# Kernel tuning notes

Measured on AMD Instinct MI355X. Metric: run time of the kernel, lower is better.

Reference implementation:

```python
import jax, jax.numpy as jnp
import numpy as np

B, U, D, N, O = 128, 16, 256, 1024, 256
RES_CONN, IN_CONN, BIAS_P = 0.2, 0.2, 0.5


def _fixed_bernoulli(rng, heads, rows, cols, conn):
    # each column has exactly nb = int(conn*rows) ones (as in the torch code)
    nb = max(1, int(conn * rows))
    r = rng.random((heads, rows, cols))
    thr = np.sort(r, axis=1)[:, nb - 1:nb, :]
    return (r <= thr).astype(np.float32)


def setup_inputs() -> dict:
    rng = np.random.default_rng(0)
    # recurrent weights: normal * fixed-bernoulli mask, normalized by spectral radius
    W = rng.normal(size=(U, N, N)).astype(np.float32) * _fixed_bernoulli(rng, U, N, N, RES_CONN)
    sr0 = np.abs(np.linalg.eigvals(W.astype(np.float64))).max(axis=-1).astype(np.float32).reshape(U, 1, 1)
    W = W / sr0
    Win = _fixed_bernoulli(rng, U, D, N, IN_CONN)
    bias = (rng.random((U, 1, N)) < BIAS_P).astype(np.float32)
    Wout = rng.normal(size=(U, N, O)).astype(np.float32)
    adaptive_lr = rng.random((U, D, 1)).astype(np.float32)
    sr = rng.random((U, 1, 1)).astype(np.float32)
    temperature = np.ones((1,), np.float32)
    X = rng.normal(size=(B, U, D)).astype(np.float32)
    state = rng.normal(size=(B, U, N)).astype(np.float32)
    arrs = dict(X=X, state=state, W=W, Win=Win, bias=bias, Wout=Wout,
                sr=sr, adaptive_lr=adaptive_lr, temperature=temperature)
    return {k: jnp.asarray(v) for k, v in arrs.items()}


def reference(X, state, W, Win, bias, Wout, sr, adaptive_lr, temperature):
    # X: [B,U,D] -> [B,U,1,D]; state: [B,U,N] -> [B,U,1,N]
    x = X[:, :, None, :]
    s = state[:, :, None, :]
    # adaptive per-unit learning rate: softmax over the units axis
    lr = jax.nn.softmax(jnp.einsum('buid,udk->buik', x, adaptive_lr) / temperature, axis=1)  # [B,U,1,1]
    feed = jnp.einsum('buid,udn->buin', x, Win)            # [B,U,1,N]
    echo = jnp.einsum('buin,unm->buim', s, W * sr) + bias  # [B,U,1,N]
    new_state = (1.0 - lr) * s + lr * jnp.tanh(feed + echo)
    output = jnp.einsum('buin,uno->buio', new_state, Wout)  # [B,U,1,O]
    return new_state[:, :, 0, :], output[:, :, 0, :]
```

## Files before the change

### kernel.cpp

```cpp
#include <hip/hip_runtime.h>
#include <math.h>

#define Bsz 128
#define Usz 16
#define Dsz 256
#define Nsz 1024
#define Osz 256

typedef __attribute__((ext_vector_type(4))) float f32x4;
typedef __attribute__((ext_vector_type(8))) short bf16x8;

__device__ __forceinline__ unsigned short f2bf(float f) {
    union { float f; unsigned int u; } v; v.f = f;
    unsigned int lsb = (v.u >> 16) & 1u;
    v.u += 0x7fffu + lsb;
    return (unsigned short)(v.u >> 16);
}

__device__ __forceinline__ bf16x8 pack8(const float* x, float s) {
    union { bf16x8 v; unsigned short h[8]; } r;
    #pragma unroll
    for (int i = 0; i < 8; i++) r.h[i] = f2bf(x[i] * s);
    return r.v;
}

__global__ __launch_bounds__(256)
void lr_kernel(const float* __restrict__ X, const float* __restrict__ alr,
               const float* __restrict__ temp, float* __restrict__ lr)
{
    const int b = blockIdx.x;
    const int t = threadIdx.x;
    const int u = t >> 4;
    const int l = t & 15;
    const float* xp = X + ((size_t)b * Usz + u) * Dsz;
    const float* ap = alr + (size_t)u * Dsz;
    float s = 0.f;
    for (int d = l; d < Dsz; d += 16) s += xp[d] * ap[d];
    s += __shfl_down(s, 8, 16);
    s += __shfl_down(s, 4, 16);
    s += __shfl_down(s, 2, 16);
    s += __shfl_down(s, 1, 16);
    __shared__ float logits[16];
    if (l == 0) logits[u] = s;
    __syncthreads();
    if (t < 16) {
        const float T = temp[0];
        float m = -1e30f;
        #pragma unroll
        for (int i = 0; i < 16; i++) m = fmaxf(m, logits[i] / T);
        float sum = 0.f;
        #pragma unroll
        for (int i = 0; i < 16; i++) sum += expf(logits[i] / T - m);
        lr[(size_t)b * Usz + t] = expf(logits[t] / T - m) / sum;
    }
}

__global__ __launch_bounds__(256)
void state_mfma(const float* __restrict__ X, const float* __restrict__ state,
                const float* __restrict__ W, const float* __restrict__ Win,
                const float* __restrict__ bias, const float* __restrict__ sr,
                const float* __restrict__ lr, float* __restrict__ out0)
{
    const int id = blockIdx.x;
    const int mt = id >> 8;
    const int rr = id & 255;
    const int u  = (rr & 7) | ((rr >> 7) << 3);
    const int nt = (rr >> 3) & 15;

    const int tid  = threadIdx.x;
    const int wave = tid >> 6, lane = tid & 63;
    const int l16  = lane & 15, kgl = lane >> 4;
    const int wrow = (wave & 1) * 32, wcol = (wave >> 1) * 32;

    __shared__ __align__(16) unsigned short As[64 * 32];
    __shared__ __align__(16) unsigned short Bs[64 * 32];

    f32x4 acc[2][2] = {};

    const int sm  = tid & 63;
    const int skg = tid >> 6;
    const float sru = sr[u];

    const float* Af = X     + ((size_t)(mt * 64 + sm) * Usz + u) * Dsz + skg * 8;
    const float* Ae = state + ((size_t)(mt * 64 + sm) * Usz + u) * Nsz + skg * 8;
    const float* Bf = Win + (size_t)u * Dsz * Nsz + (size_t)(skg * 8) * Nsz + nt * 64 + sm;
    const float* Be = W   + (size_t)u * Nsz * Nsz + (size_t)(skg * 8) * Nsz + nt * 64 + sm;

    float areg[8], breg[8];

    auto loadA = [&](int kb) {
        const float* p = (kb < Dsz) ? (Af + kb) : (Ae + (kb - Dsz));
        const f32x4 v0 = *(const f32x4*)p;
        const f32x4 v1 = *(const f32x4*)(p + 4);
        #pragma unroll
        for (int i = 0; i < 4; i++) { areg[i] = v0[i]; areg[4 + i] = v1[i]; }
    };
    auto loadB = [&](int kb) {
        const float* p = (kb < Dsz) ? (Bf + (size_t)kb * Nsz)
                                    : (Be + (size_t)(kb - Dsz) * Nsz);
        #pragma unroll
        for (int j = 0; j < 8; j++) breg[j] = p[(size_t)j * Nsz];
    };

    loadA(0); loadB(0);
    const int wr_off = ((sm >> 4) * 4 + skg) * 128 + (sm & 15) * 8;

    for (int step = 0; step < 40; ++step) {
        const int kb = step * 32;
        const float asc = (kb < Dsz) ? 1.f : sru;
        const bf16x8 av = pack8(areg, asc);
        const bf16x8 bv = pack8(breg, 1.f);
        __syncthreads();
        *(bf16x8*)&As[wr_off] = av;
        *(bf16x8*)&Bs[wr_off] = bv;
        __syncthreads();
        if (step + 1 < 40) { loadA(kb + 32); loadB(kb + 32); }
        bf16x8 afr[2], bfr[2];
        #pragma unroll
        for (int mi = 0; mi < 2; mi++)
            afr[mi] = *(const bf16x8*)&As[((((wrow >> 4) + mi) * 4 + kgl) * 16 + l16) * 8];
        #pragma unroll
        for (int ni = 0; ni < 2; ni++)
            bfr[ni] = *(const bf16x8*)&Bs[((((wcol >> 4) + ni) * 4 + kgl) * 16 + l16) * 8];
        #pragma unroll
        for (int mi = 0; mi < 2; mi++)
            #pragma unroll
            for (int ni = 0; ni < 2; ni++)
                acc[mi][ni] = __builtin_amdgcn_mfma_f32_16x16x32_bf16(afr[mi], bfr[ni], acc[mi][ni], 0, 0, 0);
    }

    #pragma unroll
    for (int mi = 0; mi < 2; mi++) {
        #pragma unroll
        for (int ni = 0; ni < 2; ni++) {
            const int gcol = nt * 64 + wcol + ni * 16 + l16;
            const float bi = bias[u * Nsz + gcol];
            #pragma unroll
            for (int rg = 0; rg < 4; rg++) {
                const int grow = mt * 64 + wrow + mi * 16 + kgl * 4 + rg;
                const size_t idx = ((size_t)grow * Usz + u) * Nsz + gcol;
                const float th = tanhf(acc[mi][ni][rg] + bi);
                const float sv = state[idx];
                const float lv = lr[grow * Usz + u];
                out0[idx] = (1.f - lv) * sv + lv * th;
            }
        }
    }
}

__global__ __launch_bounds__(256)
void out_mfma(const float* __restrict__ ns, const float* __restrict__ Wout,
              float* __restrict__ out1)
{
    const int id = blockIdx.x;
    const int u  = (id & 7) | ((id >> 7) << 3);
    const int mt = (id >> 3) & 3;
    const int ot = (id >> 5) & 3;

    const int tid  = threadIdx.x;
    const int wave = tid >> 6, lane = tid & 63;
    const int l16  = lane & 15, kgl = lane >> 4;
    const int wrow = (wave & 1) * 16, wcol = (wave >> 1) * 32;

    __shared__ __align__(16) unsigned short As[32 * 32];
    __shared__ __align__(16) unsigned short Bs[64 * 32];

    f32x4 acc[2] = {};

    const int sa_m = tid & 31, sa_kg = (tid >> 5) & 3;
    const int sb_n = tid & 63, sb_kg = tid >> 6;

    const float* Ap = ns + ((size_t)(mt * 32 + sa_m) * Usz + u) * Nsz + sa_kg * 8;
    const float* Bp = Wout + (size_t)u * Nsz * Osz + (size_t)(sb_kg * 8) * Osz + ot * 64 + sb_n;

    float areg[8], breg[8];
    auto loadA = [&](int kb) {
        if (tid < 128) {
            const f32x4 v0 = *(const f32x4*)(Ap + kb);
            const f32x4 v1 = *(const f32x4*)(Ap + kb + 4);
            #pragma unroll
            for (int i = 0; i < 4; i++) { areg[i] = v0[i]; areg[4 + i] = v1[i]; }
        }
    };
    auto loadB = [&](int kb) {
        const float* p = Bp + (size_t)kb * Osz;
        #pragma unroll
        for (int j = 0; j < 8; j++) breg[j] = p[(size_t)j * Osz];
    };

    loadA(0); loadB(0);
    const int wa_off = ((sa_m >> 4) * 4 + sa_kg) * 128 + (sa_m & 15) * 8;
    const int wb_off = ((sb_n >> 4) * 4 + sb_kg) * 128 + (sb_n & 15) * 8;

    for (int step = 0; step < 32; ++step) {
        const int kb = step * 32;
        bf16x8 av = pack8(areg, 1.f);
        const bf16x8 bv = pack8(breg, 1.f);
        __syncthreads();
        if (tid < 128) *(bf16x8*)&As[wa_off] = av;
        *(bf16x8*)&Bs[wb_off] = bv;
        __syncthreads();
        if (step + 1 < 32) { loadA(kb + 32); loadB(kb + 32); }
        const bf16x8 afr = *(const bf16x8*)&As[(((wave & 1) * 4 + kgl) * 16 + l16) * 8];
        bf16x8 bfr[2];
        #pragma unroll
        for (int ni = 0; ni < 2; ni++)
            bfr[ni] = *(const bf16x8*)&Bs[((((wcol >> 4) + ni) * 4 + kgl) * 16 + l16) * 8];
        #pragma unroll
        for (int ni = 0; ni < 2; ni++)
            acc[ni] = __builtin_amdgcn_mfma_f32_16x16x32_bf16(afr, bfr[ni], acc[ni], 0, 0, 0);
    }

    #pragma unroll
    for (int ni = 0; ni < 2; ni++) {
        const int gcol = ot * 64 + wcol + ni * 16 + l16;
        #pragma unroll
        for (int rg = 0; rg < 4; rg++) {
            const int grow = mt * 32 + wrow + kgl * 4 + rg;
            out1[((size_t)grow * Usz + u) * Osz + gcol] = acc[ni][rg];
        }
    }
}

extern "C" void kernel_launch(void* const* d_in, const int* in_sizes, int n_in,
                              void* d_out, int out_size, void* d_ws, size_t ws_size,
                              hipStream_t stream)
{
    (void)in_sizes; (void)n_in; (void)out_size; (void)ws_size;
    const float* X     = (const float*)d_in[0];
    const float* state = (const float*)d_in[1];
    const float* W     = (const float*)d_in[2];
    const float* Win   = (const float*)d_in[3];
    const float* bias  = (const float*)d_in[4];
    const float* Wout  = (const float*)d_in[5];
    const float* sr    = (const float*)d_in[6];
    const float* alr   = (const float*)d_in[7];
    const float* temp  = (const float*)d_in[8];

    float* out0 = (float*)d_out;
    float* out1 = out0 + (size_t)Bsz * Usz * Nsz;
    float* lr   = (float*)d_ws;

    lr_kernel<<<Bsz, 256, 0, stream>>>(X, alr, temp, lr);
    state_mfma<<<512, 256, 0, stream>>>(X, state, W, Win, bias, sr, lr, out0);
    out_mfma<<<256, 256, 0, stream>>>(out0, Wout, out1);
}
```

Measured before the change: 202.9 us.

## Double-buffer LDS tiles and halve M tiles to double grid size

Both MFMA GEMM kernels now use double-buffered shared memory with a two-deep register prefetch, so each step needs one barrier instead of two and global loads overlap the MFMAs. The M tile is halved (64→32 rows in the state kernel, 32→16 in the output kernel), which doubles the block count to 1024 and 512 to fill more CUs. Block-index mapping changes so units vary fastest. The trade-off is that weight tiles are re-read from global/L2 by twice as many blocks, and each wave does less MFMA work per loaded tile.

```diff
diff --git a/kernel.cpp b/kernel.cpp
--- a/kernel.cpp
+++ b/kernel.cpp
@@ -61,126 +61,128 @@
                 const float* __restrict__ bias, const float* __restrict__ sr,
                 const float* __restrict__ lr, float* __restrict__ out0)
 {
-    const int id = blockIdx.x;
-    const int mt = id >> 8;
-    const int rr = id & 255;
-    const int u  = (rr & 7) | ((rr >> 7) << 3);
-    const int nt = (rr >> 3) & 15;
-
-    const int tid  = threadIdx.x;
-    const int wave = tid >> 6, lane = tid & 63;
-    const int l16  = lane & 15, kgl = lane >> 4;
-    const int wrow = (wave & 1) * 32, wcol = (wave >> 1) * 32;
-
-    __shared__ __align__(16) unsigned short As[64 * 32];
-    __shared__ __align__(16) unsigned short Bs[64 * 32];
-
-    f32x4 acc[2][2] = {};
-
-    const int sm  = tid & 63;
-    const int skg = tid >> 6;
-    const float sru = sr[u];
-
-    const float* Af = X     + ((size_t)(mt * 64 + sm) * Usz + u) * Dsz + skg * 8;
-    const float* Ae = state + ((size_t)(mt * 64 + sm) * Usz + u) * Nsz + skg * 8;
-    const float* Bf = Win + (size_t)u * Dsz * Nsz + (size_t)(skg * 8) * Nsz + nt * 64 + sm;
-    const float* Be = W   + (size_t)u * Nsz * Nsz + (size_t)(skg * 8) * Nsz + nt * 64 + sm;
-
-    float areg[8], breg[8];
-
-    auto loadA = [&](int kb) {
-        const float* p = (kb < Dsz) ? (Af + kb) : (Ae + (kb - Dsz));
-        const f32x4 v0 = *(const f32x4*)p;
-        const f32x4 v1 = *(const f32x4*)(p + 4);
-        #pragma unroll
-        for (int i = 0; i < 4; i++) { areg[i] = v0[i]; areg[4 + i] = v1[i]; }
-    };
-    auto loadB = [&](int kb) {
-        const float* p = (kb < Dsz) ? (Bf + (size_t)kb * Nsz)
-                                    : (Be + (size_t)(kb - Dsz) * Nsz);
-        #pragma unroll
-        for (int j = 0; j < 8; j++) breg[j] = p[(size_t)j * Nsz];
-    };
-
-    loadA(0); loadB(0);
-    const int wr_off = ((sm >> 4) * 4 + skg) * 128 + (sm & 15) * 8;
-
-    for (int step = 0; step < 40; ++step) {
-        const int kb = step * 32;
-        const float asc = (kb < Dsz) ? 1.f : sru;
-        const bf16x8 av = pack8(areg, asc);
-        const bf16x8 bv = pack8(breg, 1.f);
-        __syncthreads();
-        *(bf16x8*)&As[wr_off] = av;
-        *(bf16x8*)&Bs[wr_off] = bv;
-        __syncthreads();
-        if (step + 1 < 40) { loadA(kb + 32); loadB(kb + 32); }
-        bf16x8 afr[2], bfr[2];
-        #pragma unroll
-        for (int mi = 0; mi < 2; mi++)
-            afr[mi] = *(const bf16x8*)&As[((((wrow >> 4) + mi) * 4 + kgl) * 16 + l16) * 8];
-        #pragma unroll
-        for (int ni = 0; ni < 2; ni++)
-            bfr[ni] = *(const bf16x8*)&Bs[((((wcol >> 4) + ni) * 4 + kgl) * 16 + l16) * 8];
-        #pragma unroll
-        for (int mi = 0; mi < 2; mi++)
-            #pragma unroll
-            for (int ni = 0; ni < 2; ni++)
-                acc[mi][ni] = __builtin_amdgcn_mfma_f32_16x16x32_bf16(afr[mi], bfr[ni], acc[mi][ni], 0, 0, 0);
-    }
-
-    #pragma unroll
-    for (int mi = 0; mi < 2; mi++) {
-        #pragma unroll
-        for (int ni = 0; ni < 2; ni++) {
-            const int gcol = nt * 64 + wcol + ni * 16 + l16;
-            const float bi = bias[u * Nsz + gcol];
-            #pragma unroll
-            for (int rg = 0; rg < 4; rg++) {
-                const int grow = mt * 64 + wrow + mi * 16 + kgl * 4 + rg;
-                const size_t idx = ((size_t)grow * Usz + u) * Nsz + gcol;
-                const float th = tanhf(acc[mi][ni][rg] + bi);
-                const float sv = state[idx];
-                const float lv = lr[grow * Usz + u];
-                out0[idx] = (1.f - lv) * sv + lv * th;
-            }
-        }
-    }
-}
-
-__global__ __launch_bounds__(256)
-void out_mfma(const float* __restrict__ ns, const float* __restrict__ Wout,
-              float* __restrict__ out1)
-{
-    const int id = blockIdx.x;
-    const int u  = (id & 7) | ((id >> 7) << 3);
-    const int mt = (id >> 3) & 3;
-    const int ot = (id >> 5) & 3;
+    const int id   = blockIdx.x;
+    const int u    = id & 15;
+    const int rest = id >> 4;
+    const int nt   = rest & 15;
+    const int mt   = rest >> 4;
 
     const int tid  = threadIdx.x;
     const int wave = tid >> 6, lane = tid & 63;
     const int l16  = lane & 15, kgl = lane >> 4;
     const int wrow = (wave & 1) * 16, wcol = (wave >> 1) * 32;
 
-    __shared__ __align__(16) unsigned short As[32 * 32];
-    __shared__ __align__(16) unsigned short Bs[64 * 32];
+    __shared__ __align__(16) unsigned short As[2][1024];
+    __shared__ __align__(16) unsigned short Bs[2][2048];
 
     f32x4 acc[2] = {};
 
-    const int sa_m = tid & 31, sa_kg = (tid >> 5) & 3;
-    const int sb_n = tid & 63, sb_kg = tid >> 6;
-
-    const float* Ap = ns + ((size_t)(mt * 32 + sa_m) * Usz + u) * Nsz + sa_kg * 8;
-    const float* Bp = Wout + (size_t)u * Nsz * Osz + (size_t)(sb_kg * 8) * Osz + ot * 64 + sb_n;
+    const int  sm  = tid & 31;
+    const int  skg = (tid >> 5) & 3;
+    const bool doA = tid < 128;
+    const int  sb_n = tid & 63, sb_kg = tid >> 6;
+    const float sru = sr[u];
+
+    const float* Af = X     + ((size_t)(mt * 32 + sm) * Usz + u) * Dsz + skg * 8;
+    const float* Ae = state + ((size_t)(mt * 32 + sm) * Usz + u) * Nsz + skg * 8;
+    const float* Bf = Win + (size_t)u * Dsz * Nsz + (size_t)(sb_kg * 8) * Nsz + nt * 64 + sb_n;
+    const float* Be = W   + (size_t)u * Nsz * Nsz + (size_t)(sb_kg * 8) * Nsz + nt * 64 + sb_n;
 
     float areg[8], breg[8];
     auto loadA = [&](int kb) {
-        if (tid < 128) {
-            const f32x4 v0 = *(const f32x4*)(Ap + kb);
-            const f32x4 v1 = *(const f32x4*)(Ap + kb + 4);
-            #pragma unroll
-            for (int i = 0; i < 4; i++) { areg[i] = v0[i]; areg[4 + i] = v1[i]; }
+        if (!doA) return;
+        const float* p = (kb < Dsz) ? (Af + kb) : (Ae + (kb - Dsz));
+        const f32x4 v0 = *(const f32x4*)p;
+        const f32x4 v1 = *(const f32x4*)(p + 4);
+        #pragma unroll
+        for (int i = 0; i < 4; i++) { areg[i] = v0[i]; areg[4 + i] = v1[i]; }
+    };
+    auto loadB = [&](int kb) {
+        const float* p = (kb < Dsz) ? (Bf + (size_t)kb * Nsz)
+                                    : (Be + (size_t)(kb - Dsz) * Nsz);
+        #pragma unroll
+        for (int j = 0; j < 8; j++) breg[j] = p[(size_t)j * Nsz];
+    };
+
+    const int wrA = ((sm >> 4) * 4 + skg) * 128 + (sm & 15) * 8;
+    const int wrB = ((sb_n >> 4) * 4 + sb_kg) * 128 + (sb_n & 15) * 8;
+    auto writeBuf = [&](int buf, int kb) {
+        const float asc = (kb < Dsz) ? 1.f : sru;
+        if (doA) *(bf16x8*)&As[buf][wrA] = pack8(areg, asc);
+        *(bf16x8*)&Bs[buf][wrB] = pack8(breg, 1.f);
+    };
+
+    loadA(0); loadB(0);
+    writeBuf(0, 0);
+    loadA(32); loadB(32);
+    __syncthreads();
+
+    const int aoff  = (((wave & 1) * 4 + kgl) * 16 + l16) * 8;
+    const int boff0 = ((((wcol >> 4) + 0) * 4 + kgl) * 16 + l16) * 8;
+    const int boff1 = ((((wcol >> 4) + 1) * 4 + kgl) * 16 + l16) * 8;
+
+    for (int step = 0; step < 40; ++step) {
+        const int buf = step & 1;
+        if (step + 1 < 40) writeBuf(buf ^ 1, (step + 1) * 32);
+        if (step + 2 < 40) { loadA((step + 2) * 32); loadB((step + 2) * 32); }
+        const bf16x8 afr = *(const bf16x8*)&As[buf][aoff];
+        const bf16x8 b0  = *(const bf16x8*)&Bs[buf][boff0];
+        const bf16x8 b1  = *(const bf16x8*)&Bs[buf][boff1];
+        acc[0] = __builtin_amdgcn_mfma_f32_16x16x32_bf16(afr, b0, acc[0], 0, 0, 0);
+        acc[1] = __builtin_amdgcn_mfma_f32_16x16x32_bf16(afr, b1, acc[1], 0, 0, 0);
+        __syncthreads();
+    }
+
+    #pragma unroll
+    for (int ni = 0; ni < 2; ni++) {
+        const int gcol = nt * 64 + wcol + ni * 16 + l16;
+        const float bi = bias[u * Nsz + gcol];
+        #pragma unroll
+        for (int rg = 0; rg < 4; rg++) {
+            const int grow = mt * 32 + wrow + kgl * 4 + rg;
+            const size_t idx = ((size_t)grow * Usz + u) * Nsz + gcol;
+            const float th = tanhf(acc[ni][rg] + bi);
+            const float sv = state[idx];
+            const float lv = lr[grow * Usz + u];
+            out0[idx] = (1.f - lv) * sv + lv * th;
         }
+    }
+}
+
+__global__ __launch_bounds__(256)
+void out_mfma(const float* __restrict__ ns, const float* __restrict__ Wout,
+              float* __restrict__ out1)
+{
+    const int id   = blockIdx.x;
+    const int u    = id & 15;
+    const int rest = id >> 4;
+    const int ot   = rest & 3;
+    const int mt   = rest >> 2;
+
+    const int tid  = threadIdx.x;
+    const int wave = tid >> 6, lane = tid & 63;
+    const int l16  = lane & 15, kgl = lane >> 4;
+    const int wcol = wave * 16;
+
+    __shared__ __align__(16) unsigned short As[2][512];
+    __shared__ __align__(16) unsigned short Bs[2][2048];
+
+    f32x4 acc = {};
+
+    const bool doA = tid < 64;
+    const int  sm  = tid & 15, skg = (tid >> 4) & 3;
+    const int  sb_n = tid & 63, sb_kg = tid >> 6;
+
+    const float* Ap = ns + ((size_t)(mt * 16 + sm) * Usz + u) * Nsz + skg * 8;
+    const float* Bp = Wout + (size_t)u * Nsz * Osz + (size_t)(sb_kg * 8) * Osz + ot * 64 + sb_n;
+
+    float areg[8], breg[8];
+    auto loadA = [&](int kb) {
+        if (!doA) return;
+        const f32x4 v0 = *(const f32x4*)(Ap + kb);
+        const f32x4 v1 = *(const f32x4*)(Ap + kb + 4);
+        #pragma unroll
+        for (int i = 0; i < 4; i++) { areg[i] = v0[i]; areg[4 + i] = v1[i]; }
     };
     auto loadB = [&](int kb) {
         const float* p = Bp + (size_t)kb * Osz;
@@ -188,37 +190,36 @@
         for (int j = 0; j < 8; j++) breg[j] = p[(size_t)j * Osz];
     };
 
+    const int wrA = skg * 128 + sm * 8;
+    const int wrB = ((sb_n >> 4) * 4 + sb_kg) * 128 + (sb_n & 15) * 8;
+    auto writeBuf = [&](int buf) {
+        if (doA) *(bf16x8*)&As[buf][wrA] = pack8(areg, 1.f);
+        *(bf16x8*)&Bs[buf][wrB] = pack8(breg, 1.f);
+    };
+
     loadA(0); loadB(0);
-    const int wa_off = ((sa_m >> 4) * 4 + sa_kg) * 128 + (sa_m & 15) * 8;
-    const int wb_off = ((sb_n >> 4) * 4 + sb_kg) * 128 + (sb_n & 15) * 8;
+    writeBuf(0);
+    loadA(32); loadB(32);
+    __syncthreads();
+
+    const int aoff = (kgl * 16 + l16) * 8;
+    const int boff = ((wave * 4 + kgl) * 16 + l16) * 8;
 
     for (int step = 0; step < 32; ++step) {
-        const int kb = step * 32;
-        bf16x8 av = pack8(areg, 1.f);
-        const bf16x8 bv = pack8(breg, 1.f);
+        const int buf = step & 1;
+        if (step + 1 < 32) writeBuf(buf ^ 1);
+        if (step + 2 < 32) { loadA((step + 2) * 32); loadB((step + 2) * 32); }
+        const bf16x8 afr = *(const bf16x8*)&As[buf][aoff];
+        const bf16x8 bfr = *(const bf16x8*)&Bs[buf][boff];
+        acc = __builtin_amdgcn_mfma_f32_16x16x32_bf16(afr, bfr, acc, 0, 0, 0);
         __syncthreads();
-        if (tid < 128) *(bf16x8*)&As[wa_off] = av;
-        *(bf16x8*)&Bs[wb_off] = bv;
-        __syncthreads();
-        if (step + 1 < 32) { loadA(kb + 32); loadB(kb + 32); }
-        const bf16x8 afr = *(const bf16x8*)&As[(((wave & 1) * 4 + kgl) * 16 + l16) * 8];
-        bf16x8 bfr[2];
-        #pragma unroll
-        for (int ni = 0; ni < 2; ni++)
-            bfr[ni] = *(const bf16x8*)&Bs[((((wcol >> 4) + ni) * 4 + kgl) * 16 + l16) * 8];
-        #pragma unroll
-        for (int ni = 0; ni < 2; ni++)
-            acc[ni] = __builtin_amdgcn_mfma_f32_16x16x32_bf16(afr, bfr[ni], acc[ni], 0, 0, 0);
-    }
-
+    }
+
+    const int gcol = ot * 64 + wcol + l16;
     #pragma unroll
-    for (int ni = 0; ni < 2; ni++) {
-        const int gcol = ot * 64 + wcol + ni * 16 + l16;
-        #pragma unroll
-        for (int rg = 0; rg < 4; rg++) {
-            const int grow = mt * 32 + wrow + kgl * 4 + rg;
-            out1[((size_t)grow * Usz + u) * Osz + gcol] = acc[ni][rg];
-        }
+    for (int rg = 0; rg < 4; rg++) {
+        const int grow = mt * 16 + kgl * 4 + rg;
+        out1[((size_t)grow * Usz + u) * Osz + gcol] = acc[rg];
     }
 }
 
@@ -242,6 +243,6 @@
     float* lr   = (float*)d_ws;
 
     lr_kernel<<<Bsz, 256, 0, stream>>>(X, alr, temp, lr);
-    state_mfma<<<512, 256, 0, stream>>>(X, state, W, Win, bias, sr, lr, out0);
-    out_mfma<<<256, 256, 0, stream>>>(out0, Wout, out1);
-}
+    state_mfma<<<1024, 256, 0, stream>>>(X, state, W, Win, bias, sr, lr, out0);
+    out_mfma<<<512, 256, 0, stream>>>(out0, Wout, out1);
+}
```

New measurement: 203.8 us. No clear change (+0.4%).

## Drop LDS staging in GEMM kernels, load MFMA fragments directly from global memory

Applied to the files above, without the earlier changes.

Both MFMA kernels no longer stage tiles through shared memory with two barriers per step. Each wave now loads its own A/B fragments from global memory into double-buffered registers, and conversion to bf16 becomes truncation via byte permute instead of round-to-nearest. Block-to-tile mapping changes: state_mfma puts unit in the low bits, and out_mfma gives each wave its own 16x16 tile across twice as many blocks. This removes barrier and LDS traffic but duplicates global loads across waves, and truncation lowers precision slightly.

```diff
diff --git a/kernel.cpp b/kernel.cpp
--- a/kernel.cpp
+++ b/kernel.cpp
@@ -9,19 +9,24 @@
 
 typedef __attribute__((ext_vector_type(4))) float f32x4;
 typedef __attribute__((ext_vector_type(8))) short bf16x8;
-
-__device__ __forceinline__ unsigned short f2bf(float f) {
-    union { float f; unsigned int u; } v; v.f = f;
-    unsigned int lsb = (v.u >> 16) & 1u;
-    v.u += 0x7fffu + lsb;
-    return (unsigned short)(v.u >> 16);
-}
-
-__device__ __forceinline__ bf16x8 pack8(const float* x, float s) {
-    union { bf16x8 v; unsigned short h[8]; } r;
+typedef __attribute__((ext_vector_type(4))) unsigned int u32x4;
+
+union cell_u { u32x4 u; bf16x8 b; };
+
+__device__ __forceinline__ unsigned int fbits(float f) {
+    union { float f; unsigned int u; } v; v.f = f; return v.u;
+}
+__device__ __forceinline__ unsigned int pk(float lo, float hi) {
+    return __builtin_amdgcn_perm(fbits(hi), fbits(lo), 0x07060302u);
+}
+__device__ __forceinline__ bf16x8 pk8s(const float* x, float s) {
+    float t[8];
     #pragma unroll
-    for (int i = 0; i < 8; i++) r.h[i] = f2bf(x[i] * s);
-    return r.v;
+    for (int i = 0; i < 8; i++) t[i] = x[i] * s;
+    cell_u r;
+    r.u[0] = pk(t[0], t[1]); r.u[1] = pk(t[2], t[3]);
+    r.u[2] = pk(t[4], t[5]); r.u[3] = pk(t[6], t[7]);
+    return r.b;
 }
 
 __global__ __launch_bounds__(256)
@@ -55,89 +60,93 @@
     }
 }
 
-__global__ __launch_bounds__(256)
+__global__ __launch_bounds__(256, 2)
 void state_mfma(const float* __restrict__ X, const float* __restrict__ state,
                 const float* __restrict__ W, const float* __restrict__ Win,
                 const float* __restrict__ bias, const float* __restrict__ sr,
                 const float* __restrict__ lr, float* __restrict__ out0)
 {
     const int id = blockIdx.x;
+    const int u  = id & 15;
+    const int nt = (id >> 4) & 15;
     const int mt = id >> 8;
-    const int rr = id & 255;
-    const int u  = (rr & 7) | ((rr >> 7) << 3);
-    const int nt = (rr >> 3) & 15;
 
     const int tid  = threadIdx.x;
     const int wave = tid >> 6, lane = tid & 63;
     const int l16  = lane & 15, kgl = lane >> 4;
-    const int wrow = (wave & 1) * 32, wcol = (wave >> 1) * 32;
-
-    __shared__ __align__(16) unsigned short As[64 * 32];
-    __shared__ __align__(16) unsigned short Bs[64 * 32];
+    const int wm = wave & 1, wn = wave >> 1;
+
+    const int row0 = mt * 64 + wm * 32 + l16;
+    const int col0 = nt * 64 + wn * 32 + l16;
+
+    const float sru = sr[u];
+
+    const float* Ax0 = X + ((size_t)row0 * Usz + u) * Dsz;
+    const float* Ax1 = X + ((size_t)(row0 + 16) * Usz + u) * Dsz;
+    const float* Ae0 = state + ((size_t)row0 * Usz + u) * Nsz;
+    const float* Ae1 = state + ((size_t)(row0 + 16) * Usz + u) * Nsz;
+    const float* Bf  = Win + (size_t)u * Dsz * Nsz + col0;
+    const float* Be  = W   + (size_t)u * Nsz * Nsz + col0;
+
+    float a[2][2][8];
+    float b[2][2][8];
+
+    auto loadStep = [&](int step, int buf) {
+        const int kb = step * 32 + kgl * 8;
+        if (kb < Dsz) {
+            *(f32x4*)&a[buf][0][0] = *(const f32x4*)(Ax0 + kb);
+            *(f32x4*)&a[buf][0][4] = *(const f32x4*)(Ax0 + kb + 4);
+            *(f32x4*)&a[buf][1][0] = *(const f32x4*)(Ax1 + kb);
+            *(f32x4*)&a[buf][1][4] = *(const f32x4*)(Ax1 + kb + 4);
+            const float* bp = Bf + (size_t)kb * Nsz;
+            #pragma unroll
+            for (int j = 0; j < 8; j++) {
+                b[buf][0][j] = bp[(size_t)j * Nsz];
+                b[buf][1][j] = bp[(size_t)j * Nsz + 16];
+            }
+        } else {
+            const int kk = kb - Dsz;
+            *(f32x4*)&a[buf][0][0] = *(const f32x4*)(Ae0 + kk);
+            *(f32x4*)&a[buf][0][4] = *(const f32x4*)(Ae0 + kk + 4);
+            *(f32x4*)&a[buf][1][0] = *(const f32x4*)(Ae1 + kk);
+            *(f32x4*)&a[buf][1][4] = *(const f32x4*)(Ae1 + kk + 4);
+            const float* bp = Be + (size_t)kk * Nsz;
+            #pragma unroll
+            for (int j = 0; j < 8; j++) {
+                b[buf][0][j] = bp[(size_t)j * Nsz];
+                b[buf][1][j] = bp[(size_t)j * Nsz + 16];
+            }
+        }
+    };
 
     f32x4 acc[2][2] = {};
-
-    const int sm  = tid & 63;
-    const int skg = tid >> 6;
-    const float sru = sr[u];
-
-    const float* Af = X     + ((size_t)(mt * 64 + sm) * Usz + u) * Dsz + skg * 8;
-    const float* Ae = state + ((size_t)(mt * 64 + sm) * Usz + u) * Nsz + skg * 8;
-    const float* Bf = Win + (size_t)u * Dsz * Nsz + (size_t)(skg * 8) * Nsz + nt * 64 + sm;
-    const float* Be = W   + (size_t)u * Nsz * Nsz + (size_t)(skg * 8) * Nsz + nt * 64 + sm;
-
-    float areg[8], breg[8];
-
-    auto loadA = [&](int kb) {
-        const float* p = (kb < Dsz) ? (Af + kb) : (Ae + (kb - Dsz));
-        const f32x4 v0 = *(const f32x4*)p;
-        const f32x4 v1 = *(const f32x4*)(p + 4);
-        #pragma unroll
-        for (int i = 0; i < 4; i++) { areg[i] = v0[i]; areg[4 + i] = v1[i]; }
-    };
-    auto loadB = [&](int kb) {
-        const float* p = (kb < Dsz) ? (Bf + (size_t)kb * Nsz)
-                                    : (Be + (size_t)(kb - Dsz) * Nsz);
-        #pragma unroll
-        for (int j = 0; j < 8; j++) breg[j] = p[(size_t)j * Nsz];
-    };
-
-    loadA(0); loadB(0);
-    const int wr_off = ((sm >> 4) * 4 + skg) * 128 + (sm & 15) * 8;
+    loadStep(0, 0);
 
     for (int step = 0; step < 40; ++step) {
-        const int kb = step * 32;
-        const float asc = (kb < Dsz) ? 1.f : sru;
-        const bf16x8 av = pack8(areg, asc);
-        const bf16x8 bv = pack8(breg, 1.f);
-        __syncthreads();
-        *(bf16x8*)&As[wr_off] = av;
-        *(bf16x8*)&Bs[wr_off] = bv;
-        __syncthreads();
-        if (step + 1 < 40) { loadA(kb + 32); loadB(kb + 32); }
-        bf16x8 afr[2], bfr[2];
+        const int cur = step & 1;
+        if (step + 1 < 40) loadStep(step + 1, cur ^ 1);
+        const float asc = (step < 8) ? 1.f : sru;
+        bf16x8 af[2], bf[2];
+        af[0] = pk8s(a[cur][0], asc);
+        af[1] = pk8s(a[cur][1], asc);
+        bf[0] = pk8s(b[cur][0], 1.f);
+        bf[1] = pk8s(b[cur][1], 1.f);
         #pragma unroll
         for (int mi = 0; mi < 2; mi++)
-            afr[mi] = *(const bf16x8*)&As[((((wrow >> 4) + mi) * 4 + kgl) * 16 + l16) * 8];
-        #pragma unroll
-        for (int ni = 0; ni < 2; ni++)
-            bfr[ni] = *(const bf16x8*)&Bs[((((wcol >> 4) + ni) * 4 + kgl) * 16 + l16) * 8];
-        #pragma unroll
-        for (int mi = 0; mi < 2; mi++)
             #pragma unroll
             for (int ni = 0; ni < 2; ni++)
-                acc[mi][ni] = __builtin_amdgcn_mfma_f32_16x16x32_bf16(afr[mi], bfr[ni], acc[mi][ni], 0, 0, 0);
+                acc[mi][ni] = __builtin_amdgcn_mfma_f32_16x16x32_bf16(af[mi], bf[ni], acc[mi][ni], 0, 0, 0);
     }
 
     #pragma unroll
-    for (int mi = 0; mi < 2; mi++) {
-        #pragma unroll
-        for (int ni = 0; ni < 2; ni++) {
-            const int gcol = nt * 64 + wcol + ni * 16 + l16;
-            const float bi = bias[u * Nsz + gcol];
+    for (int ni = 0; ni < 2; ni++) {
+        const int gcol = nt * 64 + wn * 32 + ni * 16 + l16;
+        const float bi = bias[u * Nsz + gcol];
+        #pragma unroll
+        for (int mi = 0; mi < 2; mi++) {
             #pragma unroll
             for (int rg = 0; rg < 4; rg++) {
-                const int grow = mt * 64 + wrow + mi * 16 + kgl * 4 + rg;
+                const int grow = mt * 64 + wm * 32 + mi * 16 + kgl * 4 + rg;
                 const size_t idx = ((size_t)grow * Usz + u) * Nsz + gcol;
                 const float th = tanhf(acc[mi][ni][rg] + bi);
                 const float sv = state[idx];
@@ -148,77 +157,46 @@
     }
 }
 
-__global__ __launch_bounds__(256)
+__global__ __launch_bounds__(256, 2)
 void out_mfma(const float* __restrict__ ns, const float* __restrict__ Wout,
               float* __restrict__ out1)
 {
-    const int id = blockIdx.x;
-    const int u  = (id & 7) | ((id >> 7) << 3);
-    const int mt = (id >> 3) & 3;
-    const int ot = (id >> 5) & 3;
-
-    const int tid  = threadIdx.x;
-    const int wave = tid >> 6, lane = tid & 63;
+    const int w  = blockIdx.x * 4 + (threadIdx.x >> 6);
+    const int u  = w & 15;
+    const int ot = (w >> 4) & 15;
+    const int mtw = w >> 8;
+
+    const int lane = threadIdx.x & 63;
     const int l16  = lane & 15, kgl = lane >> 4;
-    const int wrow = (wave & 1) * 16, wcol = (wave >> 1) * 32;
-
-    __shared__ __align__(16) unsigned short As[32 * 32];
-    __shared__ __align__(16) unsigned short Bs[64 * 32];
-
-    f32x4 acc[2] = {};
-
-    const int sa_m = tid & 31, sa_kg = (tid >> 5) & 3;
-    const int sb_n = tid & 63, sb_kg = tid >> 6;
-
-    const float* Ap = ns + ((size_t)(mt * 32 + sa_m) * Usz + u) * Nsz + sa_kg * 8;
-    const float* Bp = Wout + (size_t)u * Nsz * Osz + (size_t)(sb_kg * 8) * Osz + ot * 64 + sb_n;
-
-    float areg[8], breg[8];
-    auto loadA = [&](int kb) {
-        if (tid < 128) {
-            const f32x4 v0 = *(const f32x4*)(Ap + kb);
-            const f32x4 v1 = *(const f32x4*)(Ap + kb + 4);
-            #pragma unroll
-            for (int i = 0; i < 4; i++) { areg[i] = v0[i]; areg[4 + i] = v1[i]; }
-        }
+
+    const float* Ap = ns + ((size_t)(mtw * 16 + l16) * Usz + u) * Nsz;
+    const float* Bp = Wout + (size_t)u * Nsz * Osz + ot * 16 + l16;
+
+    float a[2][8], b[2][8];
+    auto loadStep = [&](int step, int buf) {
+        const int kb = step * 32 + kgl * 8;
+        *(f32x4*)&a[buf][0] = *(const f32x4*)(Ap + kb);
+        *(f32x4*)&a[buf][4] = *(const f32x4*)(Ap + kb + 4);
+        const float* bp = Bp + (size_t)kb * Osz;
+        #pragma unroll
+        for (int j = 0; j < 8; j++) b[buf][j] = bp[(size_t)j * Osz];
     };
-    auto loadB = [&](int kb) {
-        const float* p = Bp + (size_t)kb * Osz;
-        #pragma unroll
-        for (int j = 0; j < 8; j++) breg[j] = p[(size_t)j * Osz];
-    };
-
-    loadA(0); loadB(0);
-    const int wa_off = ((sa_m >> 4) * 4 + sa_kg) * 128 + (sa_m & 15) * 8;
-    const int wb_off = ((sb_n >> 4) * 4 + sb_kg) * 128 + (sb_n & 15) * 8;
-
+
+    f32x4 acc = {};
+    loadStep(0, 0);
     for (int step = 0; step < 32; ++step) {
-        const int kb = step * 32;
-        bf16x8 av = pack8(areg, 1.f);
-        const bf16x8 bv = pack8(breg, 1.f);
-        __syncthreads();
-        if (tid < 128) *(bf16x8*)&As[wa_off] = av;
-        *(bf16x8*)&Bs[wb_off] = bv;
-        __syncthreads();
-        if (step + 1 < 32) { loadA(kb + 32); loadB(kb + 32); }
-        const bf16x8 afr = *(const bf16x8*)&As[(((wave & 1) * 4 + kgl) * 16 + l16) * 8];
-        bf16x8 bfr[2];
-        #pragma unroll
-        for (int ni = 0; ni < 2; ni++)
-            bfr[ni] = *(const bf16x8*)&Bs[((((wcol >> 4) + ni) * 4 + kgl) * 16 + l16) * 8];
-        #pragma unroll
-        for (int ni = 0; ni < 2; ni++)
-            acc[ni] = __builtin_amdgcn_mfma_f32_16x16x32_bf16(afr, bfr[ni], acc[ni], 0, 0, 0);
-    }
-
+        const int cur = step & 1;
+        if (step + 1 < 32) loadStep(step + 1, cur ^ 1);
+        const bf16x8 af = pk8s(a[cur], 1.f);
+        const bf16x8 bf = pk8s(b[cur], 1.f);
+        acc = __builtin_amdgcn_mfma_f32_16x16x32_bf16(af, bf, acc, 0, 0, 0);
+    }
+
+    const int gcol = ot * 16 + l16;
     #pragma unroll
-    for (int ni = 0; ni < 2; ni++) {
-        const int gcol = ot * 64 + wcol + ni * 16 + l16;
-        #pragma unroll
-        for (int rg = 0; rg < 4; rg++) {
-            const int grow = mt * 32 + wrow + kgl * 4 + rg;
-            out1[((size_t)grow * Usz + u) * Osz + gcol] = acc[ni][rg];
-        }
+    for (int rg = 0; rg < 4; rg++) {
+        const int grow = mtw * 16 + kgl * 4 + rg;
+        out1[((size_t)grow * Usz + u) * Osz + gcol] = acc[rg];
     }
 }
 
@@ -243,5 +221,5 @@
 
     lr_kernel<<<Bsz, 256, 0, stream>>>(X, alr, temp, lr);
     state_mfma<<<512, 256, 0, stream>>>(X, state, W, Win, bias, sr, lr, out0);
-    out_mfma<<<256, 256, 0, stream>>>(out0, Wout, out1);
-}
+    out_mfma<<<512, 256, 0, stream>>>(out0, Wout, out1);
+}
```

Result: slower. 328.5 us (+61.9%).
